# Kernel optimization log

Measured on AMD Instinct MI355X. Metric: run time of the kernel, lower is better.

The kernel has to match this reference:

```python
import jax, jax.numpy as jnp
import numpy as np

N_NODES = 50000

def _gcn_conv(x, W, b, src, dst, num_nodes):
    # PyG GCNConv: linear transform, then D^{-1/2} A_hat D^{-1/2} aggregation (A_hat has self-loops).
    xw = x @ W                                   # [N, out]
    ones = jnp.ones(src.shape[0], dtype=x.dtype)
    deg = jax.ops.segment_sum(ones, dst, num_segments=num_nodes)  # in-degree incl. self loop
    dinv = jnp.where(deg > 0, jax.lax.rsqrt(deg), 0.0)
    norm = dinv[src] * dinv[dst]                 # [E]
    msg = xw[src] * norm[:, None]                # [E, out] gather + scale
    out = jax.ops.segment_sum(msg, dst, num_segments=num_nodes)   # scatter-add
    return out + b

def _add_self_loops(edge_index, num_nodes):
    loop = jnp.arange(num_nodes, dtype=edge_index.dtype)
    src = jnp.concatenate([edge_index[0], loop])
    dst = jnp.concatenate([edge_index[1], loop])
    return src, dst

def setup_inputs() -> dict:
    key = jax.random.key(0)
    k = jax.random.split(key, 6)
    in_dim, hid_dim, out_dim = 256, 128, 64
    n_edges = 800000
    x = jax.random.normal(k[0], (N_NODES, in_dim), dtype=jnp.float32)
    edge_index = jax.random.randint(k[1], (2, n_edges), 0, N_NODES, dtype=jnp.int64)
    W1 = jax.random.normal(k[2], (in_dim, hid_dim), dtype=jnp.float32) / np.sqrt(in_dim)
    b1 = jnp.zeros((hid_dim,), dtype=jnp.float32)
    W2 = jax.random.normal(k[3], (hid_dim, out_dim), dtype=jnp.float32) / np.sqrt(hid_dim)
    b2 = jnp.zeros((out_dim,), dtype=jnp.float32)
    return {"x": x, "edge_index": edge_index, "W1": W1, "b1": b1, "W2": W2, "b2": b2}

def reference(x, edge_index, W1, b1, W2, b2):
    src, dst = _add_self_loops(edge_index, N_NODES)
    h = jnp.tanh(_gcn_conv(x, W1, b1, src, dst, N_NODES))
    out = _gcn_conv(h, W2, b2, src, dst, N_NODES)
    return out
```

## Files before the change

kernel.cpp:

```cpp
#include <hip/hip_runtime.h>

#define INDIM 256
#define HID 128
#define OUTD 64
#define BINSHIFT 8
#define MAXBIN 256

typedef _Float16 f16x8 __attribute__((ext_vector_type(8)));
typedef float    f32x4 __attribute__((ext_vector_type(4)));

__global__ __launch_bounds__(256) void k_hist_setup(const int* __restrict__ dst, int* __restrict__ bin_counts,
                                                    int E,
                                                    const float* __restrict__ W1, const float* __restrict__ W2,
                                                    _Float16* __restrict__ W1t, _Float16* __restrict__ W2t) {
    __shared__ int h[MAXBIN];
    int tid = threadIdx.x;
    h[tid] = 0;
    __syncthreads();
    int base = blockIdx.x * 4096;
#pragma unroll
    for (int i = 0; i < 16; i++) {
        int e = base + i * 256 + tid;
        if (e < E) atomicAdd(&h[dst[e] >> BINSHIFT], 1);
    }
    __syncthreads();
    int v = h[tid];
    if (v) atomicAdd(&bin_counts[tid], v);

    constexpr int NW1 = HID * INDIM;
    constexpr int NW2 = OUTD * HID;
    int id = blockIdx.x * 256 + tid;
    if (id < NW1) {
        int n = id / INDIM, k = id % INDIM;
        W1t[id] = (_Float16)W1[k * HID + n];
    } else if (id < NW1 + NW2) {
        int j = id - NW1;
        int n = j / HID, k = j % HID;
        W2t[j] = (_Float16)W2[k * OUTD + n];
    }
}

struct __align__(16) GemmSh { _Float16 As[128][40]; _Float16 Bs[128][40]; };
struct FillSh { int h[256]; int s[256]; int rb[256]; };
struct CsrSh  { int A[256]; int B[256]; int C[256]; };
union FillU { FillSh f; GemmSh g; };
union CsrU  { CsrSh  c; GemmSh g; };

template <int BN, int K, typename AT>
__device__ __forceinline__ void gemm_body(const AT* __restrict__ X, const _Float16* __restrict__ Wt,
                                          _Float16* __restrict__ XW, int M, int rb,
                                          _Float16 (*As)[40], _Float16 (*Bs)[40])
{
    constexpr int NT = BN / 16;
    const int tid  = threadIdx.x;
    const int wave = tid >> 6;
    const int lane = tid & 63;
    const int m    = lane & 15;
    const int q    = lane >> 4;

    f32x4 acc[2][NT];
#pragma unroll
    for (int r = 0; r < 2; r++)
#pragma unroll
        for (int t = 0; t < NT; t++) acc[r][t] = (f32x4){0.f, 0.f, 0.f, 0.f};

    for (int kt = 0; kt < K; kt += 32) {
        if (kt) __syncthreads();
        if constexpr (sizeof(AT) == 4) {
#pragma unroll
            for (int i = 0; i < 4; i++) {
                int ch = tid + i * 256;
                int row = ch >> 3, c4 = ch & 7, gr = rb + row;
                float4 v = make_float4(0.f, 0.f, 0.f, 0.f);
                if (gr < M) v = *(const float4*)((const float*)X + (long)gr * K + kt + c4 * 4);
                _Float16* p = &As[row][c4 * 4];
                p[0] = (_Float16)v.x; p[1] = (_Float16)v.y;
                p[2] = (_Float16)v.z; p[3] = (_Float16)v.w;
            }
        } else {
#pragma unroll
            for (int i = 0; i < 2; i++) {
                int ch = tid + i * 256;
                int row = ch >> 2, c8 = ch & 3, gr = rb + row;
                uint4 v = make_uint4(0u, 0u, 0u, 0u);
                if (gr < M) v = *(const uint4*)((const _Float16*)X + (long)gr * K + kt + c8 * 8);
                *(uint4*)(&As[row][c8 * 8]) = v;
            }
        }
#pragma unroll
        for (int i = 0; i < BN / 64; i++) {
            int ch = tid + i * 256;
            int n = ch >> 2, c8 = ch & 3;
            *(uint4*)(&Bs[n][c8 * 8]) = *(const uint4*)(Wt + (long)n * K + kt + c8 * 8);
        }
        __syncthreads();

        f16x8 a0 = *(const f16x8*)(&As[wave * 32 + m][q * 8]);
        f16x8 a1 = *(const f16x8*)(&As[wave * 32 + 16 + m][q * 8]);
#pragma unroll
        for (int t = 0; t < NT; t++) {
            f16x8 bf = *(const f16x8*)(&Bs[t * 16 + m][q * 8]);
            acc[0][t] = __builtin_amdgcn_mfma_f32_16x16x32_f16(a0, bf, acc[0][t], 0, 0, 0);
            acc[1][t] = __builtin_amdgcn_mfma_f32_16x16x32_f16(a1, bf, acc[1][t], 0, 0, 0);
        }
    }

#pragma unroll
    for (int r2 = 0; r2 < 2; r2++) {
        int row0 = rb + wave * 32 + r2 * 16 + q * 4;
#pragma unroll
        for (int rr = 0; rr < 4; rr++) {
            int row = row0 + rr;
            if (row < M) {
#pragma unroll
                for (int t = 0; t < NT; t++)
                    XW[(long)row * BN + t * 16 + m] = (_Float16)acc[r2][t][rr];
            }
        }
    }
}

__device__ __forceinline__ void fill_body(const int* __restrict__ src, const int* __restrict__ dst,
                                          const int* __restrict__ bin_counts, int* __restrict__ bin_cursor,
                                          int* __restrict__ binned, int E, FillSh& sh)
{
    int tid = threadIdx.x;
    sh.h[tid] = 0;
    int v = bin_counts[tid];
    sh.s[tid] = v;
    __syncthreads();
    int base = blockIdx.x * 2048;
    int ep[8], eb[8], rk[8];
#pragma unroll
    for (int i = 0; i < 8; i++) {
        int e = base + i * 256 + tid;
        if (e < E) {
            int s = src[e], d = dst[e];
            ep[i] = (s << 8) | (d & 255);
            eb[i] = d >> BINSHIFT;
            rk[i] = atomicAdd(&sh.h[eb[i]], 1);
        } else {
            eb[i] = -1;
        }
    }
#pragma unroll
    for (int off = 1; off < 256; off <<= 1) {
        int t = (tid >= off) ? sh.s[tid - off] : 0;
        __syncthreads();
        sh.s[tid] += t;
        __syncthreads();
    }
    int c = sh.h[tid];
    if (c) sh.rb[tid] = (sh.s[tid] - v) + atomicAdd(&bin_cursor[tid], c);
    __syncthreads();
#pragma unroll
    for (int i = 0; i < 8; i++) {
        if (eb[i] >= 0) binned[sh.rb[eb[i]] + rk[i]] = ep[i];
    }
}

__device__ __forceinline__ void csr_body(const int* __restrict__ binned, const int* __restrict__ bin_counts,
                                         int* __restrict__ row_start, float* __restrict__ dinv,
                                         int* __restrict__ edge_src, int M, int E, CsrSh& sh)
{
    int b = blockIdx.x, tid = threadIdx.x;
    int v = bin_counts[tid];
    sh.A[tid] = v;
    __syncthreads();
#pragma unroll
    for (int off = 1; off < 256; off <<= 1) {
        int t = (tid >= off) ? sh.A[tid - off] : 0;
        __syncthreads();
        sh.A[tid] += t;
        __syncthreads();
    }
    sh.B[tid] = sh.A[tid] - v;
    __syncthreads();
    int beg = sh.B[b];
    int end = (b + 1 < 256) ? sh.B[b + 1] : E;
    if (b == 0 && tid == 0) row_start[M] = E;

    sh.A[tid] = 0;
    __syncthreads();
    for (int i = beg + tid; i < end; i += 256) {
        atomicAdd(&sh.A[binned[i] & 255], 1);
    }
    __syncthreads();
    int c = sh.A[tid];
    sh.B[tid] = c;
    __syncthreads();
#pragma unroll
    for (int off = 1; off < 256; off <<= 1) {
        int t = (tid >= off) ? sh.B[tid - off] : 0;
        __syncthreads();
        sh.B[tid] += t;
        __syncthreads();
    }
    int start = beg + sh.B[tid] - c;
    int node = (b << BINSHIFT) + tid;
    if (node < M) {
        row_start[node] = start;
        dinv[node] = rsqrtf(1.0f + (float)c);
    }
    sh.C[tid] = start;
    __syncthreads();
    for (int i = beg + tid; i < end; i += 256) {
        int p = binned[i];
        int pos = atomicAdd(&sh.C[p & 255], 1);
        edge_src[pos] = p >> 8;
    }
}

__global__ __launch_bounds__(256) void k_binfill_gemm(
    const int* __restrict__ src, const int* __restrict__ dst,
    const int* __restrict__ bin_counts, int* __restrict__ bin_cursor, int* __restrict__ binned, int E,
    const float* __restrict__ X, const _Float16* __restrict__ W1t, _Float16* __restrict__ XW, int M,
    int nfill, int rbofs)
{
    __shared__ FillU u;
    if ((int)blockIdx.x < nfill)
        fill_body(src, dst, bin_counts, bin_cursor, binned, E, u.f);
    else
        gemm_body<HID, INDIM, float>(X, W1t, XW, M, (rbofs + (int)blockIdx.x - nfill) * 128, u.g.As, u.g.Bs);
}

__global__ __launch_bounds__(256) void k_csr_gemm(
    const int* __restrict__ binned, const int* __restrict__ bin_counts,
    int* __restrict__ row_start, float* __restrict__ dinv, int* __restrict__ edge_src, int M, int E,
    const float* __restrict__ X, const _Float16* __restrict__ W1t, _Float16* __restrict__ XW,
    int nbin, int rbofs)
{
    __shared__ CsrU u;
    if ((int)blockIdx.x < nbin)
        csr_body(binned, bin_counts, row_start, dinv, edge_src, M, E, u.c);
    else
        gemm_body<HID, INDIM, float>(X, W1t, XW, M, (rbofs + (int)blockIdx.x - nbin) * 128, u.g.As, u.g.Bs);
}

__global__ __launch_bounds__(256) void k_agg1_gemm2(
    const int* __restrict__ row_start, const int* __restrict__ edge_src,
    const _Float16* __restrict__ feat,
    const float* __restrict__ bias,
    const float* __restrict__ dinv,
    const _Float16* __restrict__ W2t,
    _Float16* __restrict__ hw16, int M)
{
    constexpr int F = HID;
    __shared__ __align__(16) _Float16 Hs[16][136];
    __shared__ float Ds[16];

    const int tid = threadIdx.x;
    const int nl  = tid >> 4;
    const int c   = tid & 15;
    const int n   = blockIdx.x * 16 + nl;

    float r[8];
    float di = 0.f;
    if (n < M) {
        di = dinv[n];
        int beg = row_start[n], end = row_start[n + 1];
        f16x8 self = *(const f16x8*)(feat + (long)n * F + c * 8);
        float acc[8], acc2[8];
#pragma unroll
        for (int k = 0; k < 8; k++) { acc[k] = di * (float)self[k]; acc2[k] = 0.f; }

        int j = beg;
        for (; j + 7 < end; j += 8) {
            int s0 = edge_src[j],     s1 = edge_src[j + 1];
            int s2 = edge_src[j + 2], s3 = edge_src[j + 3];
            int s4 = edge_src[j + 4], s5 = edge_src[j + 5];
            int s6 = edge_src[j + 6], s7 = edge_src[j + 7];
            float d0 = dinv[s0], d1 = dinv[s1], d2 = dinv[s2], d3 = dinv[s3];
            float d4 = dinv[s4], d5 = dinv[s5], d6 = dinv[s6], d7 = dinv[s7];
            f16x8 v0 = *(const f16x8*)(feat + (long)s0 * F + c * 8);
            f16x8 v1 = *(const f16x8*)(feat + (long)s1 * F + c * 8);
            f16x8 v2 = *(const f16x8*)(feat + (long)s2 * F + c * 8);
            f16x8 v3 = *(const f16x8*)(feat + (long)s3 * F + c * 8);
            f16x8 v4 = *(const f16x8*)(feat + (long)s4 * F + c * 8);
            f16x8 v5 = *(const f16x8*)(feat + (long)s5 * F + c * 8);
            f16x8 v6 = *(const f16x8*)(feat + (long)s6 * F + c * 8);
            f16x8 v7 = *(const f16x8*)(feat + (long)s7 * F + c * 8);
#pragma unroll
            for (int k = 0; k < 8; k++) {
                acc[k]  = fmaf(d0, (float)v0[k], acc[k]);
                acc2[k] = fmaf(d1, (float)v1[k], acc2[k]);
                acc[k]  = fmaf(d2, (float)v2[k], acc[k]);
                acc2[k] = fmaf(d3, (float)v3[k], acc2[k]);
                acc[k]  = fmaf(d4, (float)v4[k], acc[k]);
                acc2[k] = fmaf(d5, (float)v5[k], acc2[k]);
                acc[k]  = fmaf(d6, (float)v6[k], acc[k]);
                acc2[k] = fmaf(d7, (float)v7[k], acc2[k]);
            }
        }
        for (; j + 3 < end; j += 4) {
            int s0 = edge_src[j],     s1 = edge_src[j + 1];
            int s2 = edge_src[j + 2], s3 = edge_src[j + 3];
            float d0 = dinv[s0], d1 = dinv[s1], d2 = dinv[s2], d3 = dinv[s3];
            f16x8 v0 = *(const f16x8*)(feat + (long)s0 * F + c * 8);
            f16x8 v1 = *(const f16x8*)(feat + (long)s1 * F + c * 8);
            f16x8 v2 = *(const f16x8*)(feat + (long)s2 * F + c * 8);
            f16x8 v3 = *(const f16x8*)(feat + (long)s3 * F + c * 8);
#pragma unroll
            for (int k = 0; k < 8; k++) {
                acc[k]  = fmaf(d0, (float)v0[k], acc[k]);
                acc2[k] = fmaf(d1, (float)v1[k], acc2[k]);
                acc[k]  = fmaf(d2, (float)v2[k], acc[k]);
                acc2[k] = fmaf(d3, (float)v3[k], acc2[k]);
            }
        }
        for (; j < end; j++) {
            int s = edge_src[j];
            float d = dinv[s];
            f16x8 v = *(const f16x8*)(feat + (long)s * F + c * 8);
#pragma unroll
            for (int k = 0; k < 8; k++) acc[k] = fmaf(d, (float)v[k], acc[k]);
        }

#pragma unroll
        for (int k = 0; k < 8; k++) r[k] = tanhf(bias[c * 8 + k] + di * (acc[k] + acc2[k]));
    } else {
#pragma unroll
        for (int k = 0; k < 8; k++) r[k] = 0.f;
    }

    f16x8 hh;
#pragma unroll
    for (int k = 0; k < 8; k++) hh[k] = (_Float16)r[k];
    *(f16x8*)(&Hs[nl][c * 8]) = hh;
    if (c == 0) Ds[nl] = di;
    __syncthreads();

    const int wave = tid >> 6;
    const int lane = tid & 63;
    const int m    = lane & 15;
    const int q    = lane >> 4;
    const _Float16* Wb = W2t + (long)(wave * 16 + m) * HID;

    f32x4 acc = (f32x4){0.f, 0.f, 0.f, 0.f};
#pragma unroll
    for (int kt = 0; kt < HID; kt += 32) {
        f16x8 af = *(const f16x8*)(&Hs[m][kt + q * 8]);
        f16x8 bf = *(const f16x8*)(Wb + kt + q * 8);
        acc = __builtin_amdgcn_mfma_f32_16x16x32_f16(af, bf, acc, 0, 0, 0);
    }
#pragma unroll
    for (int rr = 0; rr < 4; rr++) {
        int nl2 = q * 4 + rr;
        int row = blockIdx.x * 16 + nl2;
        if (row < M)
            hw16[(long)row * OUTD + wave * 16 + m] = (_Float16)(acc[rr] * Ds[nl2]);
    }
}

template <int F>
__global__ __launch_bounds__(256) void k_agg2(const int* __restrict__ row_start,
                                              const int* __restrict__ edge_src,
                                              const _Float16* __restrict__ feat,
                                              const float* __restrict__ bias,
                                              const float* __restrict__ dinv,
                                              float* __restrict__ out, int M) {
    constexpr int LPN = F / 8;
    constexpr int NPB = 256 / LPN;
    int n = blockIdx.x * NPB + threadIdx.x / LPN;
    int c = threadIdx.x % LPN;
    if (n >= M) return;
    int beg = row_start[n], end = row_start[n + 1];

    f16x8 self = *(const f16x8*)(feat + (long)n * F + c * 8);
    float acc[8], acc2[8];
#pragma unroll
    for (int k = 0; k < 8; k++) { acc[k] = (float)self[k]; acc2[k] = 0.f; }

    int j = beg;
    for (; j + 7 < end; j += 8) {
        int s0 = edge_src[j],     s1 = edge_src[j + 1];
        int s2 = edge_src[j + 2], s3 = edge_src[j + 3];
        int s4 = edge_src[j + 4], s5 = edge_src[j + 5];
        int s6 = edge_src[j + 6], s7 = edge_src[j + 7];
        f16x8 v0 = *(const f16x8*)(feat + (long)s0 * F + c * 8);
        f16x8 v1 = *(const f16x8*)(feat + (long)s1 * F + c * 8);
        f16x8 v2 = *(const f16x8*)(feat + (long)s2 * F + c * 8);
        f16x8 v3 = *(const f16x8*)(feat + (long)s3 * F + c * 8);
        f16x8 v4 = *(const f16x8*)(feat + (long)s4 * F + c * 8);
        f16x8 v5 = *(const f16x8*)(feat + (long)s5 * F + c * 8);
        f16x8 v6 = *(const f16x8*)(feat + (long)s6 * F + c * 8);
        f16x8 v7 = *(const f16x8*)(feat + (long)s7 * F + c * 8);
#pragma unroll
        for (int k = 0; k < 8; k++) {
            acc[k]  += (float)v0[k] + (float)v1[k];
            acc2[k] += (float)v2[k] + (float)v3[k];
            acc[k]  += (float)v4[k] + (float)v5[k];
            acc2[k] += (float)v6[k] + (float)v7[k];
        }
    }
    for (; j + 3 < end; j += 4) {
        int s0 = edge_src[j],     s1 = edge_src[j + 1];
        int s2 = edge_src[j + 2], s3 = edge_src[j + 3];
        f16x8 v0 = *(const f16x8*)(feat + (long)s0 * F + c * 8);
        f16x8 v1 = *(const f16x8*)(feat + (long)s1 * F + c * 8);
        f16x8 v2 = *(const f16x8*)(feat + (long)s2 * F + c * 8);
        f16x8 v3 = *(const f16x8*)(feat + (long)s3 * F + c * 8);
#pragma unroll
        for (int k = 0; k < 8; k++) {
            acc[k]  += (float)v0[k] + (float)v1[k];
            acc2[k] += (float)v2[k] + (float)v3[k];
        }
    }
    for (; j < end; j++) {
        int s = edge_src[j];
        f16x8 v = *(const f16x8*)(feat + (long)s * F + c * 8);
#pragma unroll
        for (int k = 0; k < 8; k++) acc[k] += (float)v[k];
    }

    float di = dinv[n];
    float r[8];
#pragma unroll
    for (int k = 0; k < 8; k++) r[k] = bias[c * 8 + k] + di * (acc[k] + acc2[k]);
    f32x4 o0 = {r[0], r[1], r[2], r[3]};
    f32x4 o1 = {r[4], r[5], r[6], r[7]};
    float* p = out + (long)n * F + c * 8;
    __builtin_nontemporal_store(o0, (f32x4*)p);
    __builtin_nontemporal_store(o1, (f32x4*)(p + 4));
}

extern "C" void kernel_launch(void* const* d_in, const int* in_sizes, int n_in,
                              void* d_out, int out_size, void* d_ws, size_t ws_size,
                              hipStream_t stream) {
    const float* x  = (const float*)d_in[0];
    const int*   ei = (const int*)d_in[1];
    const float* W1 = (const float*)d_in[2];
    const float* b1 = (const float*)d_in[3];
    const float* W2 = (const float*)d_in[4];
    const float* b2 = (const float*)d_in[5];
    float* out = (float*)d_out;

    const int M = in_sizes[0] / INDIM;
    const int E = in_sizes[1] / 2;
    const int* srcp = ei;
    const int* dstp = ei + E;

    const int Mp   = (M + 63) & ~63;
    const int NBIN = (M + 255) >> BINSHIFT;

    float*     dinv       = (float*)d_ws;
    int*       row_start  = (int*)(dinv + Mp);
    int*       bin_cursor = row_start + Mp;
    int*       bin_counts = bin_cursor + MAXBIN;
    _Float16*  W1t        = (_Float16*)(bin_counts + MAXBIN);
    _Float16*  W2t        = W1t + HID * INDIM;
    int*       binned     = (int*)(W2t + OUTD * HID);
    int*       edge_src   = binned + E;
    _Float16*  xw16       = (_Float16*)(edge_src + E);
    _Float16*  hw16       = xw16 + (long)M * HID;

    const int NWH = (E + 4095) / 4096;
    const int NWF = (E + 2047) / 2048;
    const int GB  = (M + 127) / 128;
    const int GA  = GB / 3;
    const int GBc = GB - GA;

    hipMemsetAsync(bin_cursor, 0, 2 * MAXBIN * sizeof(int), stream);
    k_hist_setup<<<NWH, 256, 0, stream>>>(dstp, bin_counts, E, W1, W2, W1t, W2t);
    k_binfill_gemm<<<NWF + GA, 256, 0, stream>>>(srcp, dstp, bin_counts, bin_cursor, binned, E,
                                                 x, W1t, xw16, M, NWF, 0);
    k_csr_gemm<<<NBIN + GBc, 256, 0, stream>>>(binned, bin_counts, row_start, dinv, edge_src, M, E,
                                               x, W1t, xw16, NBIN, GA);

    k_agg1_gemm2<<<(M + 15) / 16, 256, 0, stream>>>(row_start, edge_src, xw16, b1, dinv, W2t, hw16, M);

    k_agg2<OUTD><<<(M + 31) / 32, 256, 0, stream>>>(row_start, edge_src, hw16, b2, dinv, out, M);
}
```

Before: 224.1 us.

## Sort nodes by degree within bins to balance aggregation work

While building the CSR, each bin block now counting-sorts its 256 nodes by descending in-degree and writes a node permutation. Both aggregation kernels walk nodes in this permuted order, so threads and waves in a block handle nodes of similar degree. The aim is to cut wave divergence and idle lanes from degree imbalance in the gather loops. In exchange it adds an indirection, a small scan in the CSR kernel, and scattered output rows in the gemm2 store and in agg2.

```diff
diff --git a/kernel.cpp b/kernel.cpp
--- a/kernel.cpp
+++ b/kernel.cpp
@@ -42,7 +42,7 @@
 
 struct __align__(16) GemmSh { _Float16 As[128][40]; _Float16 Bs[128][40]; };
 struct FillSh { int h[256]; int s[256]; int rb[256]; };
-struct CsrSh  { int A[256]; int B[256]; int C[256]; };
+struct CsrSh  { int A[256]; int B[256]; int C[256]; int D[256]; int E2[256]; };
 union FillU { FillSh f; GemmSh g; };
 union CsrU  { CsrSh  c; GemmSh g; };
 
@@ -161,7 +161,8 @@
 
 __device__ __forceinline__ void csr_body(const int* __restrict__ binned, const int* __restrict__ bin_counts,
                                          int* __restrict__ row_start, float* __restrict__ dinv,
-                                         int* __restrict__ edge_src, int M, int E, CsrSh& sh)
+                                         int* __restrict__ edge_src, int* __restrict__ perm,
+                                         int M, int E, CsrSh& sh)
 {
     int b = blockIdx.x, tid = threadIdx.x;
     int v = bin_counts[tid];
@@ -202,6 +203,27 @@
         row_start[node] = start;
         dinv[node] = rsqrtf(1.0f + (float)c);
     }
+
+    sh.D[tid] = 0;
+    __syncthreads();
+    int bucket = 63 - (c < 63 ? c : 63);
+    int rk = 0;
+    if (node < M) rk = atomicAdd(&sh.D[bucket], 1);
+    __syncthreads();
+    sh.E2[tid] = (tid < 64) ? sh.D[tid] : 0;
+    __syncthreads();
+#pragma unroll
+    for (int off = 1; off < 64; off <<= 1) {
+        int t = (tid >= off) ? sh.E2[tid - off] : 0;
+        __syncthreads();
+        sh.E2[tid] += t;
+        __syncthreads();
+    }
+    if (node < M) {
+        int pbase = sh.E2[bucket] - sh.D[bucket];
+        perm[(b << 8) + pbase + rk] = node;
+    }
+
     sh.C[tid] = start;
     __syncthreads();
     for (int i = beg + tid; i < end; i += 256) {
@@ -226,13 +248,14 @@
 
 __global__ __launch_bounds__(256) void k_csr_gemm(
     const int* __restrict__ binned, const int* __restrict__ bin_counts,
-    int* __restrict__ row_start, float* __restrict__ dinv, int* __restrict__ edge_src, int M, int E,
+    int* __restrict__ row_start, float* __restrict__ dinv, int* __restrict__ edge_src,
+    int* __restrict__ perm, int M, int E,
     const float* __restrict__ X, const _Float16* __restrict__ W1t, _Float16* __restrict__ XW,
     int nbin, int rbofs)
 {
     __shared__ CsrU u;
     if ((int)blockIdx.x < nbin)
-        csr_body(binned, bin_counts, row_start, dinv, edge_src, M, E, u.c);
+        csr_body(binned, bin_counts, row_start, dinv, edge_src, perm, M, E, u.c);
     else
         gemm_body<HID, INDIM, float>(X, W1t, XW, M, (rbofs + (int)blockIdx.x - nbin) * 128, u.g.As, u.g.Bs);
 }
@@ -243,20 +266,23 @@
     const float* __restrict__ bias,
     const float* __restrict__ dinv,
     const _Float16* __restrict__ W2t,
+    const int* __restrict__ perm,
     _Float16* __restrict__ hw16, int M)
 {
     constexpr int F = HID;
     __shared__ __align__(16) _Float16 Hs[16][136];
     __shared__ float Ds[16];
+    __shared__ int Pr[16];
 
     const int tid = threadIdx.x;
     const int nl  = tid >> 4;
     const int c   = tid & 15;
-    const int n   = blockIdx.x * 16 + nl;
+    const int idx = blockIdx.x * 16 + nl;
+    const int n   = (idx < M) ? perm[idx] : -1;
 
     float r[8];
     float di = 0.f;
-    if (n < M) {
+    if (n >= 0) {
         di = dinv[n];
         int beg = row_start[n], end = row_start[n + 1];
         f16x8 self = *(const f16x8*)(feat + (long)n * F + c * 8);
@@ -327,7 +353,7 @@
 #pragma unroll
     for (int k = 0; k < 8; k++) hh[k] = (_Float16)r[k];
     *(f16x8*)(&Hs[nl][c * 8]) = hh;
-    if (c == 0) Ds[nl] = di;
+    if (c == 0) { Ds[nl] = di; Pr[nl] = n; }
     __syncthreads();
 
     const int wave = tid >> 6;
@@ -346,8 +372,8 @@
 #pragma unroll
     for (int rr = 0; rr < 4; rr++) {
         int nl2 = q * 4 + rr;
-        int row = blockIdx.x * 16 + nl2;
-        if (row < M)
+        int row = Pr[nl2];
+        if (row >= 0)
             hw16[(long)row * OUTD + wave * 16 + m] = (_Float16)(acc[rr] * Ds[nl2]);
     }
 }
@@ -358,12 +384,14 @@
                                               const _Float16* __restrict__ feat,
                                               const float* __restrict__ bias,
                                               const float* __restrict__ dinv,
+                                              const int* __restrict__ perm,
                                               float* __restrict__ out, int M) {
     constexpr int LPN = F / 8;
     constexpr int NPB = 256 / LPN;
-    int n = blockIdx.x * NPB + threadIdx.x / LPN;
+    int idx = blockIdx.x * NPB + threadIdx.x / LPN;
     int c = threadIdx.x % LPN;
-    if (n >= M) return;
+    if (idx >= M) return;
+    int n = perm[idx];
     int beg = row_start[n], end = row_start[n + 1];
 
     f16x8 self = *(const f16x8*)(feat + (long)n * F + c * 8);
@@ -445,7 +473,8 @@
 
     float*     dinv       = (float*)d_ws;
     int*       row_start  = (int*)(dinv + Mp);
-    int*       bin_cursor = row_start + Mp;
+    int*       perm       = row_start + Mp;
+    int*       bin_cursor = perm + Mp;
     int*       bin_counts = bin_cursor + MAXBIN;
     _Float16*  W1t        = (_Float16*)(bin_counts + MAXBIN);
     _Float16*  W2t        = W1t + HID * INDIM;
@@ -464,10 +493,10 @@
     k_hist_setup<<<NWH, 256, 0, stream>>>(dstp, bin_counts, E, W1, W2, W1t, W2t);
     k_binfill_gemm<<<NWF + GA, 256, 0, stream>>>(srcp, dstp, bin_counts, bin_cursor, binned, E,
                                                  x, W1t, xw16, M, NWF, 0);
-    k_csr_gemm<<<NBIN + GBc, 256, 0, stream>>>(binned, bin_counts, row_start, dinv, edge_src, M, E,
+    k_csr_gemm<<<NBIN + GBc, 256, 0, stream>>>(binned, bin_counts, row_start, dinv, edge_src, perm, M, E,
                                                x, W1t, xw16, NBIN, GA);
 
-    k_agg1_gemm2<<<(M + 15) / 16, 256, 0, stream>>>(row_start, edge_src, xw16, b1, dinv, W2t, hw16, M);
-
-    k_agg2<OUTD><<<(M + 31) / 32, 256, 0, stream>>>(row_start, edge_src, hw16, b2, dinv, out, M);
-}
+    k_agg1_gemm2<<<(M + 15) / 16, 256, 0, stream>>>(row_start, edge_src, xw16, b1, dinv, W2t, perm, hw16, M);
+
+    k_agg2<OUTD><<<(M + 31) / 32, 256, 0, stream>>>(row_start, edge_src, hw16, b2, dinv, perm, out, M);
+}
```

Result: no change. 228.6 us (+2.0%).

## Prescale layer-1 GEMM output by source dinv and drop per-edge dinv gathers

Applied to the files above, without the earlier changes.

Computes per-node in-degree with global atomics in the histogram kernel, so the GEMM blocks can compute dinv and fold the source-side normalization into the stored XW rows. The layer-1 aggregation then sums prescaled features directly, with no per-edge dinv loads or multiplies. This adds 800k global atomics on a per-node degree array and a larger memset. It also changes the fp16 rounding point, since features are scaled before conversion. Layer-2 aggregation (not shown) presumably still reads dinv per edge.

```diff
diff --git a/kernel.cpp b/kernel.cpp
--- a/kernel.cpp
+++ b/kernel.cpp
@@ -10,7 +10,7 @@
 typedef float    f32x4 __attribute__((ext_vector_type(4)));
 
 __global__ __launch_bounds__(256) void k_hist_setup(const int* __restrict__ dst, int* __restrict__ bin_counts,
-                                                    int E,
+                                                    int* __restrict__ deg, int E,
                                                     const float* __restrict__ W1, const float* __restrict__ W2,
                                                     _Float16* __restrict__ W1t, _Float16* __restrict__ W2t) {
     __shared__ int h[MAXBIN];
@@ -21,7 +21,11 @@
 #pragma unroll
     for (int i = 0; i < 16; i++) {
         int e = base + i * 256 + tid;
-        if (e < E) atomicAdd(&h[dst[e] >> BINSHIFT], 1);
+        if (e < E) {
+            int d = dst[e];
+            atomicAdd(&h[d >> BINSHIFT], 1);
+            atomicAdd(&deg[d], 1);
+        }
     }
     __syncthreads();
     int v = h[tid];
@@ -40,7 +44,7 @@
     }
 }
 
-struct __align__(16) GemmSh { _Float16 As[128][40]; _Float16 Bs[128][40]; };
+struct __align__(16) GemmSh { _Float16 As[128][40]; _Float16 Bs[128][40]; float Dv[128]; };
 struct FillSh { int h[256]; int s[256]; int rb[256]; };
 struct CsrSh  { int A[256]; int B[256]; int C[256]; };
 union FillU { FillSh f; GemmSh g; };
@@ -48,8 +52,8 @@
 
 template <int BN, int K, typename AT>
 __device__ __forceinline__ void gemm_body(const AT* __restrict__ X, const _Float16* __restrict__ Wt,
-                                          _Float16* __restrict__ XW, int M, int rb,
-                                          _Float16 (*As)[40], _Float16 (*Bs)[40])
+                                          const int* __restrict__ deg, float* __restrict__ dinv_g,
+                                          _Float16* __restrict__ XW, int M, int rb, GemmSh& sh)
 {
     constexpr int NT = BN / 16;
     const int tid  = threadIdx.x;
@@ -57,6 +61,16 @@
     const int lane = tid & 63;
     const int m    = lane & 15;
     const int q    = lane >> 4;
+
+    _Float16 (*As)[40] = sh.As;
+    _Float16 (*Bs)[40] = sh.Bs;
+
+    if (tid < 128) {
+        int gr = rb + tid;
+        float dv = 0.f;
+        if (gr < M) { dv = rsqrtf(1.0f + (float)deg[gr]); dinv_g[gr] = dv; }
+        sh.Dv[tid] = dv;
+    }
 
     f32x4 acc[2][NT];
 #pragma unroll
@@ -107,14 +121,15 @@
 
 #pragma unroll
     for (int r2 = 0; r2 < 2; r2++) {
-        int row0 = rb + wave * 32 + r2 * 16 + q * 4;
+        int lr0 = wave * 32 + r2 * 16 + q * 4;
 #pragma unroll
         for (int rr = 0; rr < 4; rr++) {
-            int row = row0 + rr;
+            int row = rb + lr0 + rr;
             if (row < M) {
+                float dv = sh.Dv[lr0 + rr];
 #pragma unroll
                 for (int t = 0; t < NT; t++)
-                    XW[(long)row * BN + t * 16 + m] = (_Float16)acc[r2][t][rr];
+                    XW[(long)row * BN + t * 16 + m] = (_Float16)(acc[r2][t][rr] * dv);
             }
         }
     }
@@ -160,8 +175,8 @@
 }
 
 __device__ __forceinline__ void csr_body(const int* __restrict__ binned, const int* __restrict__ bin_counts,
-                                         int* __restrict__ row_start, float* __restrict__ dinv,
-                                         int* __restrict__ edge_src, int M, int E, CsrSh& sh)
+                                         int* __restrict__ row_start, int* __restrict__ edge_src,
+                                         int M, int E, CsrSh& sh)
 {
     int b = blockIdx.x, tid = threadIdx.x;
     int v = bin_counts[tid];
@@ -198,10 +213,8 @@
     }
     int start = beg + sh.B[tid] - c;
     int node = (b << BINSHIFT) + tid;
-    if (node < M) {
-        row_start[node] = start;
-        dinv[node] = rsqrtf(1.0f + (float)c);
-    }
+    if (node < M) row_start[node] = start;
+
     sh.C[tid] = start;
     __syncthreads();
     for (int i = beg + tid; i < end; i += 256) {
@@ -214,27 +227,29 @@
 __global__ __launch_bounds__(256) void k_binfill_gemm(
     const int* __restrict__ src, const int* __restrict__ dst,
     const int* __restrict__ bin_counts, int* __restrict__ bin_cursor, int* __restrict__ binned, int E,
-    const float* __restrict__ X, const _Float16* __restrict__ W1t, _Float16* __restrict__ XW, int M,
-    int nfill, int rbofs)
+    const float* __restrict__ X, const _Float16* __restrict__ W1t,
+    const int* __restrict__ deg, float* __restrict__ dinv,
+    _Float16* __restrict__ XW, int M, int nfill, int rbofs)
 {
     __shared__ FillU u;
     if ((int)blockIdx.x < nfill)
         fill_body(src, dst, bin_counts, bin_cursor, binned, E, u.f);
     else
-        gemm_body<HID, INDIM, float>(X, W1t, XW, M, (rbofs + (int)blockIdx.x - nfill) * 128, u.g.As, u.g.Bs);
+        gemm_body<HID, INDIM, float>(X, W1t, deg, dinv, XW, M, (rbofs + (int)blockIdx.x - nfill) * 128, u.g);
 }
 
 __global__ __launch_bounds__(256) void k_csr_gemm(
     const int* __restrict__ binned, const int* __restrict__ bin_counts,
-    int* __restrict__ row_start, float* __restrict__ dinv, int* __restrict__ edge_src, int M, int E,
-    const float* __restrict__ X, const _Float16* __restrict__ W1t, _Float16* __restrict__ XW,
-    int nbin, int rbofs)
+    int* __restrict__ row_start, int* __restrict__ edge_src, int M, int E,
+    const float* __restrict__ X, const _Float16* __restrict__ W1t,
+    const int* __restrict__ deg, float* __restrict__ dinv,
+    _Float16* __restrict__ XW, int nbin, int rbofs)
 {
     __shared__ CsrU u;
     if ((int)blockIdx.x < nbin)
-        csr_body(binned, bin_counts, row_start, dinv, edge_src, M, E, u.c);
+        csr_body(binned, bin_counts, row_start, edge_src, M, E, u.c);
     else
-        gemm_body<HID, INDIM, float>(X, W1t, XW, M, (rbofs + (int)blockIdx.x - nbin) * 128, u.g.As, u.g.Bs);
+        gemm_body<HID, INDIM, float>(X, W1t, deg, dinv, XW, M, (rbofs + (int)blockIdx.x - nbin) * 128, u.g);
 }
 
 __global__ __launch_bounds__(256) void k_agg1_gemm2(
@@ -262,7 +277,7 @@
         f16x8 self = *(const f16x8*)(feat + (long)n * F + c * 8);
         float acc[8], acc2[8];
 #pragma unroll
-        for (int k = 0; k < 8; k++) { acc[k] = di * (float)self[k]; acc2[k] = 0.f; }
+        for (int k = 0; k < 8; k++) { acc[k] = (float)self[k]; acc2[k] = 0.f; }
 
         int j = beg;
         for (; j + 7 < end; j += 8) {
@@ -270,8 +285,6 @@
             int s2 = edge_src[j + 2], s3 = edge_src[j + 3];
             int s4 = edge_src[j + 4], s5 = edge_src[j + 5];
             int s6 = edge_src[j + 6], s7 = edge_src[j + 7];
-            float d0 = dinv[s0], d1 = dinv[s1], d2 = dinv[s2], d3 = dinv[s3];
-            float d4 = dinv[s4], d5 = dinv[s5], d6 = dinv[s6], d7 = dinv[s7];
             f16x8 v0 = *(const f16x8*)(feat + (long)s0 * F + c * 8);
             f16x8 v1 = *(const f16x8*)(feat + (long)s1 * F + c * 8);
             f16x8 v2 = *(const f16x8*)(feat + (long)s2 * F + c * 8);
@@ -282,38 +295,30 @@
             f16x8 v7 = *(const f16x8*)(feat + (long)s7 * F + c * 8);
 #pragma unroll
             for (int k = 0; k < 8; k++) {
-                acc[k]  = fmaf(d0, (float)v0[k], acc[k]);
-                acc2[k] = fmaf(d1, (float)v1[k], acc2[k]);
-                acc[k]  = fmaf(d2, (float)v2[k], acc[k]);
-                acc2[k] = fmaf(d3, (float)v3[k], acc2[k]);
-                acc[k]  = fmaf(d4, (float)v4[k], acc[k]);
-                acc2[k] = fmaf(d5, (float)v5[k], acc2[k]);
-                acc[k]  = fmaf(d6, (float)v6[k], acc[k]);
-                acc2[k] = fmaf(d7, (float)v7[k], acc2[k]);
+                acc[k]  += (float)v0[k] + (float)v1[k];
+                acc2[k] += (float)v2[k] + (float)v3[k];
+                acc[k]  += (float)v4[k] + (float)v5[k];
+                acc2[k] += (float)v6[k] + (float)v7[k];
             }
         }
         for (; j + 3 < end; j += 4) {
             int s0 = edge_src[j],     s1 = edge_src[j + 1];
             int s2 = edge_src[j + 2], s3 = edge_src[j + 3];
-            float d0 = dinv[s0], d1 = dinv[s1], d2 = dinv[s2], d3 = dinv[s3];
             f16x8 v0 = *(const f16x8*)(feat + (long)s0 * F + c * 8);
             f16x8 v1 = *(const f16x8*)(feat + (long)s1 * F + c * 8);
             f16x8 v2 = *(const f16x8*)(feat + (long)s2 * F + c * 8);
             f16x8 v3 = *(const f16x8*)(feat + (long)s3 * F + c * 8);
 #pragma unroll
             for (int k = 0; k < 8; k++) {
-                acc[k]  = fmaf(d0, (float)v0[k], acc[k]);
-                acc2[k] = fmaf(d1, (float)v1[k], acc2[k]);
-                acc[k]  = fmaf(d2, (float)v2[k], acc[k]);
-                acc2[k] = fmaf(d3, (float)v3[k], acc2[k]);
+                acc[k]  += (float)v0[k] + (float)v1[k];
+                acc2[k] += (float)v2[k] + (float)v3[k];
             }
         }
         for (; j < end; j++) {
             int s = edge_src[j];
-            float d = dinv[s];
             f16x8 v = *(const f16x8*)(feat + (long)s * F + c * 8);
 #pragma unroll
-            for (int k = 0; k < 8; k++) acc[k] = fmaf(d, (float)v[k], acc[k]);
+            for (int k = 0; k < 8; k++) acc[k] += (float)v[k];
         }
 
 #pragma unroll
@@ -447,7 +452,8 @@
     int*       row_start  = (int*)(dinv + Mp);
     int*       bin_cursor = row_start + Mp;
     int*       bin_counts = bin_cursor + MAXBIN;
-    _Float16*  W1t        = (_Float16*)(bin_counts + MAXBIN);
+    int*       deg        = bin_counts + MAXBIN;
+    _Float16*  W1t        = (_Float16*)(deg + Mp);
     _Float16*  W2t        = W1t + HID * INDIM;
     int*       binned     = (int*)(W2t + OUTD * HID);
     int*       edge_src   = binned + E;
@@ -460,12 +466,12 @@
     const int GA  = GB / 3;
     const int GBc = GB - GA;
 
-    hipMemsetAsync(bin_cursor, 0, 2 * MAXBIN * sizeof(int), stream);
-    k_hist_setup<<<NWH, 256, 0, stream>>>(dstp, bin_counts, E, W1, W2, W1t, W2t);
+    hipMemsetAsync(bin_cursor, 0, (2 * MAXBIN + Mp) * sizeof(int), stream);
+    k_hist_setup<<<NWH, 256, 0, stream>>>(dstp, bin_counts, deg, E, W1, W2, W1t, W2t);
     k_binfill_gemm<<<NWF + GA, 256, 0, stream>>>(srcp, dstp, bin_counts, bin_cursor, binned, E,
-                                                 x, W1t, xw16, M, NWF, 0);
-    k_csr_gemm<<<NBIN + GBc, 256, 0, stream>>>(binned, bin_counts, row_start, dinv, edge_src, M, E,
-                                               x, W1t, xw16, NBIN, GA);
+                                                 x, W1t, deg, dinv, xw16, M, NWF, 0);
+    k_csr_gemm<<<NBIN + GBc, 256, 0, stream>>>(binned, bin_counts, row_start, edge_src, M, E,
+                                               x, W1t, deg, dinv, xw16, NBIN, GA);
 
     k_agg1_gemm2<<<(M + 15) / 16, 256, 0, stream>>>(row_start, edge_src, xw16, b1, dinv, W2t, hw16, M);
 
```

New measurement: 254.1 us. +13.4%, slower.
